# Optimization experiments

Hardware: AMD Instinct MI355X
Metric: run time of the kernel (lower is better)

The kernel has to match this reference:

```python
import jax, jax.numpy as jnp
import numpy as np

N_NODES = 100000
N_EDGES = 1600000
IN_FEAT = 64
OUT_FEAT = 64


def setup_inputs() -> dict:
    key = jax.random.key(0)
    k_feat, k_src, k_dst, k_tw, k_tb, k_pw, k_pb = jax.random.split(key, 7)
    bound = 1.0 / np.sqrt(IN_FEAT)
    return {
        "feat": jax.random.normal(k_feat, (N_NODES, IN_FEAT), dtype=jnp.float32),
        "src": jax.random.randint(k_src, (N_EDGES,), 0, N_NODES, dtype=jnp.int32),
        "dst": jax.random.randint(k_dst, (N_EDGES,), 0, N_NODES, dtype=jnp.int32),
        "theta_w": jax.random.uniform(k_tw, (OUT_FEAT, IN_FEAT), jnp.float32, -bound, bound),
        "theta_b": jax.random.uniform(k_tb, (OUT_FEAT,), jnp.float32, -bound, bound),
        "phi_w": jax.random.uniform(k_pw, (OUT_FEAT, IN_FEAT), jnp.float32, -bound, bound),
        "phi_b": jax.random.uniform(k_pb, (OUT_FEAT,), jnp.float32, -bound, bound),
    }


def reference(feat, src, dst, theta_w, theta_b, phi_w, phi_b):
    # Two dense projections: h_theta = theta(feat), h_phi = phi(feat)
    h_theta = feat @ theta_w.T + theta_b          # [N, out_feat]
    h_phi = feat @ phi_w.T + phi_b                # [N, out_feat]
    diff = h_phi - h_theta                        # dstdata['x']
    # u_add_v: per-edge message e = h_theta[src] + (h_phi - h_theta)[dst]
    e = h_theta[src] + diff[dst]                  # [E, out_feat]
    # fn.max('e', 'x'): segment max over destination nodes
    out = jax.ops.segment_max(e, dst, num_segments=N_NODES)  # [N, out_feat]
    # DGL fills zero-in-degree destinations with 0 (segment_max yields -inf)
    return jnp.where(jnp.isfinite(out), out, jnp.float32(0))
```

## Files before the change

### kernel.cpp

```cpp
#include <hip/hip_runtime.h>
#include <hip/hip_bf16.h>
#include <hip/hip_fp16.h>

#define F 64
#define BSH 7
#define NBMAX 1024
#define CHUNK 4096
#define EPT 8
#define BCAP 4096
#define WPAD 72

typedef __bf16 bf16x8 __attribute__((ext_vector_type(8)));
typedef float  f32x4  __attribute__((ext_vector_type(4)));
typedef unsigned int uint4v __attribute__((ext_vector_type(4)));

__device__ inline unsigned pkmax(unsigned a, unsigned b) {
    unsigned d;
    asm volatile("v_pk_max_f16 %0, %1, %2" : "=v"(d) : "v"(a), "v"(b));
    return d;
}
__device__ inline uint4v pkmax4(uint4v a, uint4v b) {
    uint4v r;
    r.x = pkmax(a.x, b.x); r.y = pkmax(a.y, b.y);
    r.z = pkmax(a.z, b.z); r.w = pkmax(a.w, b.w);
    return r;
}
__device__ inline float half_lo(unsigned u) {
    union { unsigned short s; _Float16 h; } c; c.s = (unsigned short)(u & 0xFFFF);
    return (float)c.h;
}
__device__ inline float half_hi(unsigned u) {
    union { unsigned short s; _Float16 h; } c; c.s = (unsigned short)(u >> 16);
    return (float)c.h;
}

__global__ __launch_bounds__(256) void proj_mfma(
    const float* __restrict__ feat,
    const float* __restrict__ theta_w, const float* __restrict__ theta_b,
    const float* __restrict__ phi_w,  const float* __restrict__ phi_b,
    _Float16* __restrict__ h16, _Float16* __restrict__ d16,
    int* __restrict__ bcnt, int n_nodes)
{
    __shared__ __bf16 w2t[128 * WPAD];
    __shared__ float  bias[128];

    if (blockIdx.x == 0) {
        for (int i = threadIdx.x; i < NBMAX; i += 256) bcnt[i] = 0;
    }

    for (int i = threadIdx.x; i < 128 * 64; i += 256) {
        int n = i >> 6, k = i & 63;
        float v = (n < 64) ? theta_w[n * 64 + k]
                           : phi_w[(n - 64) * 64 + k] - theta_w[(n - 64) * 64 + k];
        w2t[n * WPAD + k] = (__bf16)v;
    }
    if (threadIdx.x < 128) {
        int n = threadIdx.x;
        bias[n] = (n < 64) ? theta_b[n] : (phi_b[n - 64] - theta_b[n - 64]);
    }
    __syncthreads();

    const int lane = threadIdx.x & 63;
    const int wv   = threadIdx.x >> 6;
    const int m    = lane & 15;
    const int q    = lane >> 4;
    const int nchunks = (n_nodes + 63) >> 6;

    for (int ch = blockIdx.x; ch < nchunks; ch += gridDim.x) {
        const int rowbase = ch * 64 + wv * 16;
        int arow = rowbase + m;
        int rs = arow < n_nodes ? arow : 0;

        bf16x8 a0, a1;
        {
            const float* p0 = feat + (size_t)rs * 64 + q * 8;
            #pragma unroll
            for (int j = 0; j < 8; ++j) a0[j] = (__bf16)p0[j];
            #pragma unroll
            for (int j = 0; j < 8; ++j) a1[j] = (__bf16)p0[32 + j];
        }

        f32x4 acc[8];
        #pragma unroll
        for (int c = 0; c < 8; ++c) acc[c] = (f32x4){0.f, 0.f, 0.f, 0.f};

        #pragma unroll
        for (int c = 0; c < 8; ++c) {
            const __bf16* wp = &w2t[(c * 16 + m) * WPAD + q * 8];
            bf16x8 b0 = *(const bf16x8*)wp;
            bf16x8 b1 = *(const bf16x8*)(wp + 32);
            acc[c] = __builtin_amdgcn_mfma_f32_16x16x32_bf16(a0, b0, acc[c], 0, 0, 0);
            acc[c] = __builtin_amdgcn_mfma_f32_16x16x32_bf16(a1, b1, acc[c], 0, 0, 0);
        }

        #pragma unroll
        for (int c = 0; c < 8; ++c) {
            float bb = bias[c * 16 + m];
            #pragma unroll
            for (int r = 0; r < 4; ++r) {
                int orow = rowbase + q * 4 + r;
                if (orow < n_nodes) {
                    float v = acc[c][r] + bb;
                    if (c < 4)
                        h16[(size_t)orow * F + c * 16 + m] = (_Float16)v;
                    else
                        d16[(size_t)orow * F + (c - 4) * 16 + m] = (_Float16)v;
                }
            }
        }
    }
}

__global__ __launch_bounds__(512) void binning_kernel(
    const int* __restrict__ src, const int* __restrict__ dst,
    int* __restrict__ bcnt, unsigned* __restrict__ packed,
    int n_edges, int nb)
{
    __shared__ int cur[NBMAX];
    __shared__ int gb[NBMAX];

    const int t = threadIdx.x;
    const int base = blockIdx.x * CHUNK;
    const int cnt = min(CHUNK, n_edges - base);

    for (int i = t; i < nb; i += 512) cur[i] = 0;
    __syncthreads();

    unsigned w[EPT];
    int      bk[EPT];
    int      rk[EPT];
    const int k0 = t * EPT;

    if (k0 + EPT <= cnt) {
        #pragma unroll
        for (int j = 0; j < EPT; ++j) {
            int k = k0 + j;
            int s = src[base + k], d = dst[base + k];
            w[j]  = ((unsigned)(d & ((1 << BSH) - 1)) << 17) | (unsigned)s;
            int b = d >> BSH;
            bk[j] = b;
            rk[j] = atomicAdd(&cur[b], 1);
        }
    } else {
        #pragma unroll
        for (int j = 0; j < EPT; ++j) {
            int k = k0 + j;
            bk[j] = -1;
            if (k < cnt) {
                int s = src[base + k], d = dst[base + k];
                w[j]  = ((unsigned)(d & ((1 << BSH) - 1)) << 17) | (unsigned)s;
                int b = d >> BSH;
                bk[j] = b;
                rk[j] = atomicAdd(&cur[b], 1);
            }
        }
    }
    __syncthreads();

    for (int i = t; i < nb; i += 512) {
        int c = cur[i];
        gb[i] = c ? atomicAdd(&bcnt[i], c) : 0;
    }
    __syncthreads();

    #pragma unroll
    for (int j = 0; j < EPT; ++j) {
        if (bk[j] >= 0) {
            int pos = gb[bk[j]] + rk[j];
            if (pos < BCAP) packed[(size_t)bk[j] * BCAP + pos] = w[j];
        }
    }
}

__global__ __launch_bounds__(256) void fine_kernel(
    const unsigned* __restrict__ packed, const int* __restrict__ bcnt,
    int* __restrict__ row_beg, int* __restrict__ row_end,
    int* __restrict__ sorted_src, int n_nodes)
{
    __shared__ int fcnt[128];
    __shared__ int fbeg[128];
    __shared__ int fs[256];

    const int b = blockIdx.x, t = threadIdx.x;
    const int beg = b * BCAP;
    const int cnt = min(bcnt[b], BCAP);

    if (t < 128) fcnt[t] = 0;
    __syncthreads();

    unsigned w[16];
    int      rk[16];
    #pragma unroll
    for (int j = 0; j < 16; ++j) {
        int k = j * 256 + t;
        rk[j] = -1;
        if (k < cnt) {
            unsigned wrd = packed[beg + k];
            w[j]  = wrd;
            rk[j] = atomicAdd(&fcnt[wrd >> 17], 1);
        }
    }
    __syncthreads();

    int v = (t < 128) ? fcnt[t] : 0;
    fs[t] = v;
    __syncthreads();
    for (int off = 1; off < 128; off <<= 1) {
        int x = (t >= off) ? fs[t - off] : 0;
        __syncthreads();
        fs[t] += x;
        __syncthreads();
    }
    if (t < 128) {
        int exc = fs[t] - v;
        int node = (b << BSH) + t;
        if (node < n_nodes) {
            row_beg[node] = beg + exc;
            row_end[node] = beg + exc + v;
        }
        fbeg[t] = beg + exc;
    }
    __syncthreads();

    #pragma unroll
    for (int j = 0; j < 16; ++j) {
        if (rk[j] >= 0) {
            int node = w[j] >> 17;
            sorted_src[fbeg[node] + rk[j]] = (int)(w[j] & 0x1FFFFu);
        }
    }
}

__global__ __launch_bounds__(256) void reduce_kernel(
    const int* __restrict__ row_beg, const int* __restrict__ row_end,
    const int* __restrict__ sorted_src,
    const _Float16* __restrict__ h16, const _Float16* __restrict__ d16,
    float* __restrict__ out, int n_nodes)
{
    const int wid  = (blockIdx.x * blockDim.x + threadIdx.x) >> 6;
    const int lane = threadIdx.x & 63;
    const int g    = lane >> 3;
    const int f8   = lane & 7;

    const int node = wid * 8 + g;
    const int nc   = node < n_nodes ? node : n_nodes - 1;

    const int beg = row_beg[nc];
    const int end = row_end[nc];
    const int deg = end - beg;
    const int last = beg + (deg > 0 ? deg - 1 : 0);

    int mdeg = deg;
    mdeg = max(mdeg, __shfl_xor(mdeg, 8));
    mdeg = max(mdeg, __shfl_xor(mdeg, 16));
    mdeg = max(mdeg, __shfl_xor(mdeg, 32));

    const unsigned NEG = 0xFC00FC00u;
    uint4v A = (uint4v){NEG, NEG, NEG, NEG};
    uint4v B = (uint4v){NEG, NEG, NEG, NEG};
    uint4v C = (uint4v){NEG, NEG, NEG, NEG};
    uint4v D = (uint4v){NEG, NEG, NEG, NEG};

    for (int e = 0; e < mdeg; e += 4) {
        int p0 = beg + e;     p0 = p0 < last ? p0 : last;
        int p1 = beg + e + 1; p1 = p1 < last ? p1 : last;
        int p2 = beg + e + 2; p2 = p2 < last ? p2 : last;
        int p3 = beg + e + 3; p3 = p3 < last ? p3 : last;
        int i0 = sorted_src[p0];
        int i1 = sorted_src[p1];
        int i2 = sorted_src[p2];
        int i3 = sorted_src[p3];
        uint4v v0 = *(const uint4v*)(h16 + (size_t)i0 * F + f8 * 8);
        uint4v v1 = *(const uint4v*)(h16 + (size_t)i1 * F + f8 * 8);
        uint4v v2 = *(const uint4v*)(h16 + (size_t)i2 * F + f8 * 8);
        uint4v v3 = *(const uint4v*)(h16 + (size_t)i3 * F + f8 * 8);
        A = pkmax4(A, v0);
        B = pkmax4(B, v1);
        C = pkmax4(C, v2);
        D = pkmax4(D, v3);
    }

    A = pkmax4(A, B);
    C = pkmax4(C, D);
    A = pkmax4(A, C);

    if (node < n_nodes) {
        size_t o = (size_t)node * F + f8 * 8;
        f32x4 r0, r1;
        if (deg > 0) {
            uint4v dv = __builtin_nontemporal_load((const uint4v*)(d16 + o));
            r0[0] = half_lo(dv.x) + half_lo(A.x);
            r0[1] = half_hi(dv.x) + half_hi(A.x);
            r0[2] = half_lo(dv.y) + half_lo(A.y);
            r0[3] = half_hi(dv.y) + half_hi(A.y);
            r1[0] = half_lo(dv.z) + half_lo(A.z);
            r1[1] = half_hi(dv.z) + half_hi(A.z);
            r1[2] = half_lo(dv.w) + half_lo(A.w);
            r1[3] = half_hi(dv.w) + half_hi(A.w);
        } else {
            r0 = (f32x4){0.f, 0.f, 0.f, 0.f};
            r1 = (f32x4){0.f, 0.f, 0.f, 0.f};
        }
        __builtin_nontemporal_store(r0, (f32x4*)(out + o));
        __builtin_nontemporal_store(r1, (f32x4*)(out + o + 4));
    }
}

extern "C" void kernel_launch(void* const* d_in, const int* in_sizes, int n_in,
                              void* d_out, int out_size, void* d_ws, size_t ws_size,
                              hipStream_t stream) {
    const float* feat    = (const float*)d_in[0];
    const int*   src     = (const int*)d_in[1];
    const int*   dst     = (const int*)d_in[2];
    const float* theta_w = (const float*)d_in[3];
    const float* theta_b = (const float*)d_in[4];
    const float* phi_w   = (const float*)d_in[5];
    const float* phi_b   = (const float*)d_in[6];
    float* out = (float*)d_out;

    const int n_nodes = in_sizes[0] / F;
    const int n_edges = in_sizes[1];
    const int nb      = (n_nodes + (1 << BSH) - 1) >> BSH;

    _Float16* h16        = (_Float16*)d_ws;
    _Float16* d16        = h16 + (size_t)n_nodes * F;
    unsigned* packed     = (unsigned*)(d16 + (size_t)n_nodes * F);
    int*      sorted_src = (int*)(packed + (size_t)nb * BCAP);
    int*      row_beg    = sorted_src + (size_t)nb * BCAP;
    int*      row_end    = row_beg + n_nodes;
    int*      bcnt       = row_end + n_nodes;

    proj_mfma<<<512, 256, 0, stream>>>(feat, theta_w, theta_b, phi_w, phi_b,
                                       h16, d16, bcnt, n_nodes);

    int bin_blocks = (n_edges + CHUNK - 1) / CHUNK;
    binning_kernel<<<bin_blocks, 512, 0, stream>>>(src, dst, bcnt, packed,
                                                   n_edges, nb);
    fine_kernel<<<nb, 256, 0, stream>>>(packed, bcnt, row_beg, row_end,
                                        sorted_src, n_nodes);

    int waves   = (n_nodes + 7) / 8;
    int rblocks = (waves * 64 + 255) / 256;
    reduce_kernel<<<rblocks, 256, 0, stream>>>(row_beg, row_end, sorted_src,
                                               h16, d16, out, n_nodes);
}
```

Baseline: 166.1 us.

## Fuse projection and edge binning into one heterogeneous kernel launch

Merges the MFMA projection kernel and the edge-binning kernel into a single launch. Block indices below bin_blocks do binning and the rest do the projection, with the shared-memory layouts overlaid in a union. The bin counter reset moves from block 0 of the projection kernel to a hipMemsetAsync. The goal is to let the two independent stages run concurrently on the GPU and to remove one launch boundary, at the cost of an extra memset and larger 512-thread projection blocks.

After: 158.5 us. 4.6% less time.

```diff
diff --git a/kernel.cpp b/kernel.cpp
--- a/kernel.cpp
+++ b/kernel.cpp
@@ -34,140 +34,137 @@
     return (float)c.h;
 }
 
-__global__ __launch_bounds__(256) void proj_mfma(
+union FusedSh {
+    struct { __bf16 w2t[128 * WPAD]; float bias[128]; } p;
+    struct { int cur[NBMAX]; int gb[NBMAX]; } b;
+};
+
+__global__ __launch_bounds__(512) void fused_proj_bin(
     const float* __restrict__ feat,
     const float* __restrict__ theta_w, const float* __restrict__ theta_b,
     const float* __restrict__ phi_w,  const float* __restrict__ phi_b,
     _Float16* __restrict__ h16, _Float16* __restrict__ d16,
-    int* __restrict__ bcnt, int n_nodes)
-{
-    __shared__ __bf16 w2t[128 * WPAD];
-    __shared__ float  bias[128];
-
-    if (blockIdx.x == 0) {
-        for (int i = threadIdx.x; i < NBMAX; i += 256) bcnt[i] = 0;
-    }
-
-    for (int i = threadIdx.x; i < 128 * 64; i += 256) {
-        int n = i >> 6, k = i & 63;
-        float v = (n < 64) ? theta_w[n * 64 + k]
-                           : phi_w[(n - 64) * 64 + k] - theta_w[(n - 64) * 64 + k];
-        w2t[n * WPAD + k] = (__bf16)v;
-    }
-    if (threadIdx.x < 128) {
-        int n = threadIdx.x;
-        bias[n] = (n < 64) ? theta_b[n] : (phi_b[n - 64] - theta_b[n - 64]);
-    }
-    __syncthreads();
-
-    const int lane = threadIdx.x & 63;
-    const int wv   = threadIdx.x >> 6;
-    const int m    = lane & 15;
-    const int q    = lane >> 4;
-    const int nchunks = (n_nodes + 63) >> 6;
-
-    for (int ch = blockIdx.x; ch < nchunks; ch += gridDim.x) {
-        const int rowbase = ch * 64 + wv * 16;
-        int arow = rowbase + m;
-        int rs = arow < n_nodes ? arow : 0;
-
-        bf16x8 a0, a1;
-        {
-            const float* p0 = feat + (size_t)rs * 64 + q * 8;
-            #pragma unroll
-            for (int j = 0; j < 8; ++j) a0[j] = (__bf16)p0[j];
-            #pragma unroll
-            for (int j = 0; j < 8; ++j) a1[j] = (__bf16)p0[32 + j];
-        }
-
-        f32x4 acc[8];
-        #pragma unroll
-        for (int c = 0; c < 8; ++c) acc[c] = (f32x4){0.f, 0.f, 0.f, 0.f};
-
-        #pragma unroll
-        for (int c = 0; c < 8; ++c) {
-            const __bf16* wp = &w2t[(c * 16 + m) * WPAD + q * 8];
-            bf16x8 b0 = *(const bf16x8*)wp;
-            bf16x8 b1 = *(const bf16x8*)(wp + 32);
-            acc[c] = __builtin_amdgcn_mfma_f32_16x16x32_bf16(a0, b0, acc[c], 0, 0, 0);
-            acc[c] = __builtin_amdgcn_mfma_f32_16x16x32_bf16(a1, b1, acc[c], 0, 0, 0);
-        }
-
-        #pragma unroll
-        for (int c = 0; c < 8; ++c) {
-            float bb = bias[c * 16 + m];
-            #pragma unroll
-            for (int r = 0; r < 4; ++r) {
-                int orow = rowbase + q * 4 + r;
-                if (orow < n_nodes) {
-                    float v = acc[c][r] + bb;
-                    if (c < 4)
-                        h16[(size_t)orow * F + c * 16 + m] = (_Float16)v;
-                    else
-                        d16[(size_t)orow * F + (c - 4) * 16 + m] = (_Float16)v;
-                }
-            }
-        }
-    }
-}
-
-__global__ __launch_bounds__(512) void binning_kernel(
     const int* __restrict__ src, const int* __restrict__ dst,
     int* __restrict__ bcnt, unsigned* __restrict__ packed,
-    int n_edges, int nb)
+    int n_nodes, int n_edges, int nb, int bin_blocks, int proj_blocks)
 {
-    __shared__ int cur[NBMAX];
-    __shared__ int gb[NBMAX];
-
+    __shared__ FusedSh sh;
     const int t = threadIdx.x;
-    const int base = blockIdx.x * CHUNK;
-    const int cnt = min(CHUNK, n_edges - base);
-
-    for (int i = t; i < nb; i += 512) cur[i] = 0;
-    __syncthreads();
-
-    unsigned w[EPT];
-    int      bk[EPT];
-    int      rk[EPT];
-    const int k0 = t * EPT;
-
-    if (k0 + EPT <= cnt) {
-        #pragma unroll
-        for (int j = 0; j < EPT; ++j) {
-            int k = k0 + j;
-            int s = src[base + k], d = dst[base + k];
-            w[j]  = ((unsigned)(d & ((1 << BSH) - 1)) << 17) | (unsigned)s;
-            int b = d >> BSH;
-            bk[j] = b;
-            rk[j] = atomicAdd(&cur[b], 1);
-        }
-    } else {
-        #pragma unroll
-        for (int j = 0; j < EPT; ++j) {
-            int k = k0 + j;
-            bk[j] = -1;
-            if (k < cnt) {
+
+    if (blockIdx.x < bin_blocks) {
+        const int base = blockIdx.x * CHUNK;
+        const int cnt = min(CHUNK, n_edges - base);
+
+        for (int i = t; i < nb; i += 512) sh.b.cur[i] = 0;
+        __syncthreads();
+
+        unsigned w[EPT];
+        int      bk[EPT];
+        int      rk[EPT];
+        const int k0 = t * EPT;
+
+        if (k0 + EPT <= cnt) {
+            #pragma unroll
+            for (int j = 0; j < EPT; ++j) {
+                int k = k0 + j;
                 int s = src[base + k], d = dst[base + k];
                 w[j]  = ((unsigned)(d & ((1 << BSH) - 1)) << 17) | (unsigned)s;
                 int b = d >> BSH;
                 bk[j] = b;
-                rk[j] = atomicAdd(&cur[b], 1);
-            }
-        }
-    }
-    __syncthreads();
-
-    for (int i = t; i < nb; i += 512) {
-        int c = cur[i];
-        gb[i] = c ? atomicAdd(&bcnt[i], c) : 0;
-    }
-    __syncthreads();
-
-    #pragma unroll
-    for (int j = 0; j < EPT; ++j) {
-        if (bk[j] >= 0) {
-            int pos = gb[bk[j]] + rk[j];
-            if (pos < BCAP) packed[(size_t)bk[j] * BCAP + pos] = w[j];
+                rk[j] = atomicAdd(&sh.b.cur[b], 1);
+            }
+        } else {
+            #pragma unroll
+            for (int j = 0; j < EPT; ++j) {
+                int k = k0 + j;
+                bk[j] = -1;
+                if (k < cnt) {
+                    int s = src[base + k], d = dst[base + k];
+                    w[j]  = ((unsigned)(d & ((1 << BSH) - 1)) << 17) | (unsigned)s;
+                    int b = d >> BSH;
+                    bk[j] = b;
+                    rk[j] = atomicAdd(&sh.b.cur[b], 1);
+                }
+            }
+        }
+        __syncthreads();
+
+        for (int i = t; i < nb; i += 512) {
+            int c = sh.b.cur[i];
+            sh.b.gb[i] = c ? atomicAdd(&bcnt[i], c) : 0;
+        }
+        __syncthreads();
+
+        #pragma unroll
+        for (int j = 0; j < EPT; ++j) {
+            if (bk[j] >= 0) {
+                int pos = sh.b.gb[bk[j]] + rk[j];
+                if (pos < BCAP) packed[(size_t)bk[j] * BCAP + pos] = w[j];
+            }
+        }
+    } else {
+        const int pb = blockIdx.x - bin_blocks;
+
+        for (int i = t; i < 128 * 64; i += 512) {
+            int n = i >> 6, k = i & 63;
+            float v = (n < 64) ? theta_w[n * 64 + k]
+                               : phi_w[(n - 64) * 64 + k] - theta_w[(n - 64) * 64 + k];
+            sh.p.w2t[n * WPAD + k] = (__bf16)v;
+        }
+        if (t < 128) {
+            int n = t;
+            sh.p.bias[n] = (n < 64) ? theta_b[n] : (phi_b[n - 64] - theta_b[n - 64]);
+        }
+        __syncthreads();
+
+        const int lane = t & 63;
+        const int wv   = t >> 6;
+        const int m    = lane & 15;
+        const int q    = lane >> 4;
+        const int nchunks = (n_nodes + 127) >> 7;
+
+        for (int ch = pb; ch < nchunks; ch += proj_blocks) {
+            const int rowbase = ch * 128 + wv * 16;
+            int arow = rowbase + m;
+            int rs = arow < n_nodes ? arow : 0;
+
+            bf16x8 a0, a1;
+            {
+                const float* p0 = feat + (size_t)rs * 64 + q * 8;
+                #pragma unroll
+                for (int j = 0; j < 8; ++j) a0[j] = (__bf16)p0[j];
+                #pragma unroll
+                for (int j = 0; j < 8; ++j) a1[j] = (__bf16)p0[32 + j];
+            }
+
+            f32x4 acc[8];
+            #pragma unroll
+            for (int c = 0; c < 8; ++c) acc[c] = (f32x4){0.f, 0.f, 0.f, 0.f};
+
+            #pragma unroll
+            for (int c = 0; c < 8; ++c) {
+                const __bf16* wp = &sh.p.w2t[(c * 16 + m) * WPAD + q * 8];
+                bf16x8 b0 = *(const bf16x8*)wp;
+                bf16x8 b1 = *(const bf16x8*)(wp + 32);
+                acc[c] = __builtin_amdgcn_mfma_f32_16x16x32_bf16(a0, b0, acc[c], 0, 0, 0);
+                acc[c] = __builtin_amdgcn_mfma_f32_16x16x32_bf16(a1, b1, acc[c], 0, 0, 0);
+            }
+
+            #pragma unroll
+            for (int c = 0; c < 8; ++c) {
+                float bb = sh.p.bias[c * 16 + m];
+                #pragma unroll
+                for (int r = 0; r < 4; ++r) {
+                    int orow = rowbase + q * 4 + r;
+                    if (orow < n_nodes) {
+                        float v = acc[c][r] + bb;
+                        if (c < 4)
+                            h16[(size_t)orow * F + c * 16 + m] = (_Float16)v;
+                        else
+                            d16[(size_t)orow * F + (c - 4) * 16 + m] = (_Float16)v;
+                    }
+                }
+            }
         }
     }
 }
@@ -330,12 +327,14 @@
     int*      row_end    = row_beg + n_nodes;
     int*      bcnt       = row_end + n_nodes;
 
-    proj_mfma<<<512, 256, 0, stream>>>(feat, theta_w, theta_b, phi_w, phi_b,
-                                       h16, d16, bcnt, n_nodes);
-
-    int bin_blocks = (n_edges + CHUNK - 1) / CHUNK;
-    binning_kernel<<<bin_blocks, 512, 0, stream>>>(src, dst, bcnt, packed,
-                                                   n_edges, nb);
+    hipMemsetAsync(bcnt, 0, NBMAX * sizeof(int), stream);
+
+    const int bin_blocks  = (n_edges + CHUNK - 1) / CHUNK;
+    const int proj_blocks = 391;
+    fused_proj_bin<<<bin_blocks + proj_blocks, 512, 0, stream>>>(
+        feat, theta_w, theta_b, phi_w, phi_b, h16, d16,
+        src, dst, bcnt, packed, n_nodes, n_edges, nb, bin_blocks, proj_blocks);
+
     fine_kernel<<<nb, 256, 0, stream>>>(packed, bcnt, row_beg, row_end,
                                         sorted_src, n_nodes);
 
```
